# Kernel optimization log

Measured on AMD Instinct MI355X. Metric: run time of the kernel, lower is better.

Reference implementation:

```python
import jax, jax.numpy as jnp
import numpy as np

# 8 fully-diagonal directions, same order as the torch list comprehension
DIRS = [(i, j, k) for i in (-1, 1) for j in (-1, 1) for k in (-1, 1)]


def conv3d(x, w, b):
    # x: (B,Cin,D,H,W), w: (Cout,Cin,3,3,3), padding=1, stride=1
    y = jax.lax.conv_general_dilated(
        x, w, window_strides=(1, 1, 1), padding=[(1, 1)] * 3,
        dimension_numbers=('NCDHW', 'OIDHW', 'NCDHW'))
    return y + b[None, :, None, None, None]


def gru_diag_scan(z, hb, h0):
    """GruDirection3d.forward_3 with d=(1,1,1) (inputs already flipped).
    O[i,j,k] = z[i,j,k]*hb[i,j,k] + (1-z[i,j,k])*P, P = h0 if min(i,j,k)==0 else O[i-1,j-1,k-1].
    Implemented exactly as the original three slab updates per step (static slices)."""
    B, C, D, H, W = z.shape
    h = jnp.broadcast_to(h0[None, :, None, None, None].astype(z.dtype),
                         (B, C, D + 1, H + 1, W + 1))
    for ti in range(min(D, H, W)):
        a = z[:, :, ti, ti:, ti:]; g = hb[:, :, ti, ti:, ti:]
        h = h.at[:, :, ti + 1, ti + 1:, ti + 1:].set(a * g + (1 - a) * h[:, :, ti, ti:H, ti:W])
        a = z[:, :, ti + 1:, ti, ti:]; g = hb[:, :, ti + 1:, ti, ti:]
        h = h.at[:, :, ti + 2:, ti + 1, ti + 1:].set(a * g + (1 - a) * h[:, :, ti + 1:D, ti, ti:W])
        a = z[:, :, ti + 1:, ti + 1:, ti]; g = hb[:, :, ti + 1:, ti + 1:, ti]
        h = h.at[:, :, ti + 2:, ti + 2:, ti + 1].set(a * g + (1 - a) * h[:, :, ti + 1:D, ti + 1:H, ti])
    return h[:, :, 1:, 1:, 1:]


def setup_inputs() -> dict:
    key = jax.random.key(0)
    ks = jax.random.split(key, 8)
    B, Cin, Cout, D = 2, 32, 32, 32
    x = jax.random.normal(ks[0], (B, Cin, D, D, D), dtype=jnp.float32)
    s = 0.05  # keep conv pre-activations in a sane range for the sigmoids
    Wh = s * jax.random.normal(ks[1], (8, Cout, Cin, 3, 3, 3), dtype=jnp.float32)
    bh = s * jax.random.normal(ks[2], (8, Cout), dtype=jnp.float32)
    Wz = s * jax.random.normal(ks[3], (8, Cout, Cin, 3, 3, 3), dtype=jnp.float32)
    bz = s * jax.random.normal(ks[4], (8, Cout), dtype=jnp.float32)
    Ws = s * jax.random.normal(ks[5], (8, Cout, Cin, 3, 3, 3), dtype=jnp.float32)
    bs = s * jax.random.normal(ks[6], (8, Cout), dtype=jnp.float32)
    h0 = s * jax.random.normal(ks[7], (8, Cout), dtype=jnp.float32)
    return {"x": x, "Wh": Wh, "bh": bh, "Wz": Wz, "bz": bz, "Ws": Ws, "bs": bs, "h0": h0}


def reference(x, Wh, bh, Wz, bz, Ws, bs, h0):
    out = None
    for n, (di, dj, dk) in enumerate(DIRS):
        hb = conv3d(x, Wh[n], bh[n])
        z = jax.nn.sigmoid(conv3d(x, Wz[n], bz[n]))
        s = jax.nn.sigmoid(conv3d(x, Ws[n], bs[n]))
        flip_axes = tuple(ax for ax, d in zip((2, 3, 4), (di, dj, dk)) if d < 0)
        zf = jnp.flip(z, flip_axes) if flip_axes else z
        hf = jnp.flip(hb, flip_axes) if flip_axes else hb
        hout = gru_diag_scan(zf, hf, h0[n])
        hout = jnp.flip(hout, flip_axes) if flip_axes else hout
        contrib = hout * s
        out = contrib if out is None else out + contrib
    return out
```

## Files before the change

kernel.cpp:

```cpp
#include <hip/hip_runtime.h>
#include <hip/hip_bf16.h>
#include <math.h>

#define NB 2
#define NC 32
#define DD 32
#define VOL (DD*DD*DD)
#define WDIR (NC*NC*27)
#define BUF_ELEMS (NB*VOL*NC)
#define WT_DIR (27*96*32)

typedef __attribute__((ext_vector_type(8))) short short8;
typedef __attribute__((ext_vector_type(4))) float f32x4;

__device__ __forceinline__ short f2bf(float v) {
    unsigned u = __float_as_uint(v);
    unsigned r = (u + 0x7fffu + ((u >> 16) & 1u)) >> 16;
    return (short)r;
}
__device__ __forceinline__ float bf2f(short s) {
    return __uint_as_float(((unsigned)(unsigned short)s) << 16);
}
__device__ __forceinline__ float bf2f_lo(unsigned u) {
    return __uint_as_float(u << 16);
}
__device__ __forceinline__ float bf2f_hi(unsigned u) {
    return __uint_as_float(u & 0xffff0000u);
}
__device__ __forceinline__ unsigned pack2(float a, float b) {
    return ((unsigned)(unsigned short)f2bf(a)) | (((unsigned)(unsigned short)f2bf(b)) << 16);
}

__device__ __forceinline__ void async_copy16(const void* g, void* l) {
    __builtin_amdgcn_global_load_lds(
        (const __attribute__((address_space(1))) unsigned*)g,
        (__attribute__((address_space(3))) unsigned*)l, 16, 0, 0);
}

__global__ __launch_bounds__(256) void prep_xw(
    const float* __restrict__ x,
    const float* __restrict__ Wh, const float* __restrict__ Wz,
    const float* __restrict__ Ws,
    short* __restrict__ xT, short* __restrict__ Wt)
{
    __shared__ float tl[32][33];
    if (blockIdx.x < 2048) {
        const int blk = blockIdx.x;
        const int b = blk >> 10;
        const int i = (blk >> 5) & 31;
        const int j = blk & 31;

        const int k  = threadIdx.x & 31;
        const int cq = threadIdx.x >> 5;
        #pragma unroll
        for (int t = 0; t < 4; ++t) {
            const int ci = cq * 4 + t;
            tl[ci][k] = x[(((b*NC + ci)*DD + i)*DD + j)*DD + k];
        }
        __syncthreads();
        const int ci2 = threadIdx.x & 31;
        const int kq  = threadIdx.x >> 5;
        const int base = ((b*DD + i)*DD + j)*DD*NC;
        #pragma unroll
        for (int t = 0; t < 4; ++t) {
            const int kk = kq * 4 + t;
            xT[base + kk*NC + ci2] = f2bf(tl[ci2][kk]);
        }
    } else {
        const int idx = (blockIdx.x - 2048) * 256 + threadIdx.x;
        if (idx >= 8*WT_DIR) return;
        const int ci  = idx & 31;
        const int n   = (idx >> 5) % 96;
        const int tap = (idx / (96*32)) % 27;
        const int dir = idx / WT_DIR;
        const int g   = n >> 5;
        const int co  = n & 31;
        const float* W = (g == 0) ? Wh : (g == 1) ? Wz : Ws;
        Wt[idx] = f2bf(W[dir*WDIR + (co*NC + ci)*27 + tap]);
    }
}

__global__ __launch_bounds__(256, 3) void conv_mfma(
    const short* __restrict__ xT, const short* __restrict__ Wt,
    const float* __restrict__ bh, const float* __restrict__ bz,
    const float* __restrict__ bs,
    short* __restrict__ bufh, short* __restrict__ bufz, short* __restrict__ bufs)
{
    __shared__ __align__(16) short As[18*34*32];

    const int tid  = threadIdx.x;
    const int lane = tid & 63;
    const int wave = tid >> 6;
    const int mh   = wave & 1;
    const int nh   = wave >> 1;
    const int lr   = lane & 15;
    const int lq   = lane >> 4;

    const int blk = blockIdx.x;
    const int j0  = (blk & 7) * 4;
    const int i   = (blk >> 3) & 31;
    const int b   = (blk >> 8) & 1;
    const int dir = blk >> 9;

    if (tid < 144) {
        const int row = tid >> 3;
        const int e   = tid & 7;
        const int off = row*2176 + (e < 4 ? e*16 : 2112 + (e - 4)*16);
        *(short8*)((char*)As + off) = short8{};
    }
    for (int t = wave; t < 36; t += 4) {
        const int row  = t >> 1;
        const int half = t & 1;
        const int rr = row / 6, jc = row - rr*6;
        const int ii = i + rr - 1, jj = j0 + jc - 1;
        char* ldst = (char*)As + row*2176 + 64 + half*1024 + lane*16;
        if ((unsigned)ii < 32u && (unsigned)jj < 32u) {
            const char* g = (const char*)(xT + ((b*DD + ii)*DD + jj)*DD*NC)
                            + half*1024 + lane*16;
            async_copy16(g, ldst);
        } else {
            *(short8*)ldst = short8{};
        }
    }
    __syncthreads();

    const int nbase = nh*48;
    const short* __restrict__ Wd = Wt + dir*WT_DIR;

    f32x4 acc[4][3];
    #pragma unroll
    for (int nt = 0; nt < 3; ++nt) {
        #pragma unroll
        for (int r = 0; r < 4; ++r) {
            const int n = nbase + nt*16 + lq*4 + r;
            const int gg = n >> 5, co = n & 31;
            const float bv = (gg == 0) ? bh[dir*NC + co]
                           : (gg == 1) ? bz[dir*NC + co] : bs[dir*NC + co];
            #pragma unroll
            for (int mt = 0; mt < 4; ++mt) acc[mt][nt][r] = bv;
        }
    }

    #pragma unroll
    for (int g9 = 0; g9 < 9; ++g9) {
        short8 bfr[3][3];
        #pragma unroll
        for (int rk = 0; rk < 3; ++rk)
            #pragma unroll
            for (int nt = 0; nt < 3; ++nt)
                bfr[rk][nt] = *(const short8*)
                    &Wd[((g9*3 + rk)*96 + nbase + nt*16 + lr)*32 + lq*8];

        const int ri = g9 / 3;
        const int rj = g9 - 3*ri;
        const int rowb = (ri*6 + mh*2 + rj) * 1088;

        #pragma unroll
        for (int rk = 0; rk < 3; ++rk) {
            short8 afr[4];
            #pragma unroll
            for (int mt = 0; mt < 4; ++mt) {
                const int jd  = mt >> 1;
                const int kvr = (mt & 1)*16 + lr + rk;
                afr[mt] = *(const short8*)&As[rowb + jd*1088 + kvr*32 + lq*8];
            }
            #pragma unroll
            for (int mt = 0; mt < 4; ++mt)
                #pragma unroll
                for (int nt = 0; nt < 3; ++nt)
                    acc[mt][nt] = __builtin_amdgcn_mfma_f32_16x16x32_bf16(
                        bfr[rk][nt], afr[mt], acc[mt][nt], 0, 0, 0);
        }
    }

    #pragma unroll
    for (int nt = 0; nt < 3; ++nt) {
        const int n0 = nbase + nt*16 + lq*4;
        const int gg = n0 >> 5;
        const int co = n0 & 31;
        short* __restrict__ dst = ((gg == 0) ? bufh : (gg == 1) ? bufz : bufs)
                                  + (size_t)dir * BUF_ELEMS;
        #pragma unroll
        for (int mt = 0; mt < 4; ++mt) {
            const int jd = mt >> 1;
            const int kv = (mt & 1)*16 + lr;
            float v0 = acc[mt][nt][0], v1 = acc[mt][nt][1];
            float v2 = acc[mt][nt][2], v3 = acc[mt][nt][3];
            if (gg != 0) {
                v0 = 1.0f/(1.0f + __expf(-v0)); v1 = 1.0f/(1.0f + __expf(-v1));
                v2 = 1.0f/(1.0f + __expf(-v2)); v3 = 1.0f/(1.0f + __expf(-v3));
            }
            uint2 pk = { pack2(v0, v1), pack2(v2, v3) };
            *(uint2*)&dst[((((b*DD + i)*DD + (j0 + mh*2 + jd))*DD + kv)*NC) + co] = pk;
        }
    }
}

__global__ __launch_bounds__(256) void gru_scan(
    const short* __restrict__ bufh, const short* __restrict__ bufz,
    const short* __restrict__ bufs, short* __restrict__ cont,
    const float* __restrict__ h0)
{
    const int dir = blockIdx.z;
    const int di = (dir & 4) ? 1 : -1;
    const int dj = (dir & 2) ? 1 : -1;
    const int dk = (dir & 1) ? 1 : -1;
    const size_t doff = (size_t)dir * BUF_ELEMS;
    const short* __restrict__ bh_ = bufh + doff;
    const short* __restrict__ bz_ = bufz + doff;
    const short* __restrict__ bs_ = bufs + doff;
    short* __restrict__ ct_ = cont + doff;

    const int c8   = threadIdx.x & 7;
    const int slot = threadIdx.x >> 3;
    const int cid  = blockIdx.x * 32 + slot;
    if (cid >= 2977) return;
    const int b = blockIdx.y;

    int ic, jc, kc;
    if (cid < 1024)      { ic = 0;             jc = cid >> 5;      kc = cid & 31; }
    else if (cid < 2016) { int t = cid - 1024; ic = 1 + (t >> 5);  jc = 0; kc = t & 31; }
    else                 { int t = cid - 2016; int q = t / 31;
                           ic = 1 + q;         jc = 1 + (t - q*31); kc = 0; }

    int mx = ic > jc ? ic : jc; if (kc > mx) mx = kc;
    const int L  = 32 - mx;
    const int i0 = (di > 0) ? ic : 31 - ic;
    const int j0 = (dj > 0) ? jc : 31 - jc;
    const int k0 = (dk > 0) ? kc : 31 - kc;
    const int step = di*(DD*DD*NC) + dj*(DD*NC) + dk*NC;

    int p = b*(VOL*NC) + i0*(DD*DD*NC) + j0*(DD*NC) + k0*NC + c8*4;
    float p0 = h0[dir*NC + c8*4 + 0];
    float p1 = h0[dir*NC + c8*4 + 1];
    float p2 = h0[dir*NC + c8*4 + 2];
    float p3 = h0[dir*NC + c8*4 + 3];

    for (int s = 0; s < L; ++s) {
        const uint2 uz = *(const uint2*)&bz_[p];
        const uint2 uh = *(const uint2*)&bh_[p];
        const uint2 us = *(const uint2*)&bs_[p];

        const float z0 = bf2f_lo(uz.x), z1 = bf2f_hi(uz.x);
        const float z2 = bf2f_lo(uz.y), z3 = bf2f_hi(uz.y);
        const float h0v = bf2f_lo(uh.x), h1v = bf2f_hi(uh.x);
        const float h2v = bf2f_lo(uh.y), h3v = bf2f_hi(uh.y);
        const float s0 = bf2f_lo(us.x), s1 = bf2f_hi(us.x);
        const float s2 = bf2f_lo(us.y), s3 = bf2f_hi(us.y);

        const float o0 = z0*h0v + (1.0f - z0)*p0;
        const float o1 = z1*h1v + (1.0f - z1)*p1;
        const float o2 = z2*h2v + (1.0f - z2)*p2;
        const float o3 = z3*h3v + (1.0f - z3)*p3;

        uint2 pk = { pack2(o0*s0, o1*s1), pack2(o2*s2, o3*s3) };
        *(uint2*)&ct_[p] = pk;

        p0 = o0; p1 = o1; p2 = o2; p3 = o3;
        p += step;
    }
}

__global__ __launch_bounds__(256) void transpose_out(
    const short* __restrict__ contrib, float* __restrict__ out)
{
    __shared__ float tl[32][33];
    const int blk = blockIdx.x;
    const int b = blk >> 10;
    const int i = (blk >> 5) & 31;
    const int j = blk & 31;

    const int c  = threadIdx.x & 31;
    const int kq = threadIdx.x >> 5;
    const int base = ((b*DD + i)*DD + j)*DD*NC;
    #pragma unroll
    for (int t = 0; t < 4; ++t) {
        const int k = kq*4 + t;
        float s = 0.0f;
        #pragma unroll
        for (int d = 0; d < 8; ++d)
            s += bf2f(contrib[(size_t)d*BUF_ELEMS + base + k*NC + c]);
        tl[k][c] = s;
    }
    __syncthreads();

    const int k2 = threadIdx.x & 31;
    const int cq = threadIdx.x >> 5;
    const int obase = b*(NC*VOL) + i*(DD*DD) + j*DD;
    #pragma unroll
    for (int t = 0; t < 4; ++t) {
        const int co = cq*4 + t;
        out[obase + co*VOL + k2] = tl[k2][co];
    }
}

extern "C" void kernel_launch(void* const* d_in, const int* in_sizes, int n_in,
                              void* d_out, int out_size, void* d_ws, size_t ws_size,
                              hipStream_t stream)
{
    const float* x  = (const float*)d_in[0];
    const float* Wh = (const float*)d_in[1];
    const float* bh = (const float*)d_in[2];
    const float* Wz = (const float*)d_in[3];
    const float* bz = (const float*)d_in[4];
    const float* Ws = (const float*)d_in[5];
    const float* bs = (const float*)d_in[6];
    const float* h0 = (const float*)d_in[7];
    float* out = (float*)d_out;

    short* bufh = (short*)d_ws;
    short* bufz = bufh + 8*(size_t)BUF_ELEMS;
    short* bufs = bufz + 8*(size_t)BUF_ELEMS;
    short* xT   = bufs + 8*(size_t)BUF_ELEMS;
    short* Wt   = xT + BUF_ELEMS;
    short* cont = Wt + 8*(size_t)WT_DIR;

    prep_xw<<<2048 + (8*WT_DIR + 255)/256, 256, 0, stream>>>(x, Wh, Wz, Ws, xT, Wt);

    conv_mfma<<<8*NB*DD*8, 256, 0, stream>>>(xT, Wt, bh, bz, bs, bufh, bufz, bufs);

    gru_scan<<<dim3((2977 + 31)/32, NB, 8), 256, 0, stream>>>(bufh, bufz, bufs, cont, h0);

    transpose_out<<<NB*DD*DD, 256, 0, stream>>>(cont, out);
}
```

Baseline: 213.0 us.

## Switch conv to 32x32x16 MFMA with 2x4 row tiles and swizzled LDS

The implicit-GEMM conv now uses 32x32x16 bf16 MFMA instead of 16x16x32. Each block covers two i-rows by four j-rows, with each wave owning two rows across all 96 output channels. The halo tile in LDS grows to 24 rows and uses an XOR swizzle on the 16-byte chunks to avoid bank conflicts. The aim is more weight and input reuse per block and fewer halo loads per output, at the cost of more accumulator registers and a halved grid that may reduce occupancy.

After: 216.2 us. Within noise of the previous version (+1.5%).

```diff
diff --git a/kernel.cpp b/kernel.cpp
--- a/kernel.cpp
+++ b/kernel.cpp
@@ -11,7 +11,7 @@
 #define WT_DIR (27*96*32)
 
 typedef __attribute__((ext_vector_type(8))) short short8;
-typedef __attribute__((ext_vector_type(4))) float f32x4;
+typedef __attribute__((ext_vector_type(16))) float f32x16;
 
 __device__ __forceinline__ short f2bf(float v) {
     unsigned u = __float_as_uint(v);
@@ -86,112 +86,112 @@
     const float* __restrict__ bs,
     short* __restrict__ bufh, short* __restrict__ bufz, short* __restrict__ bufs)
 {
-    __shared__ __align__(16) short As[18*34*32];
+    __shared__ __align__(16) short As[24*34*32];
 
     const int tid  = threadIdx.x;
     const int lane = tid & 63;
-    const int wave = tid >> 6;
-    const int mh   = wave & 1;
-    const int nh   = wave >> 1;
-    const int lr   = lane & 15;
-    const int lq   = lane >> 4;
+    const int w    = tid >> 6;
+    const int kv   = lane & 31;
+    const int hl   = lane >> 5;
 
     const int blk = blockIdx.x;
     const int j0  = (blk & 7) * 4;
-    const int i   = (blk >> 3) & 31;
-    const int b   = (blk >> 8) & 1;
-    const int dir = blk >> 9;
-
-    if (tid < 144) {
+    const int i0  = ((blk >> 3) & 15) * 2;
+    const int b   = (blk >> 7) & 1;
+    const int dir = blk >> 8;
+
+    if (tid < 192) {
         const int row = tid >> 3;
         const int e   = tid & 7;
-        const int off = row*2176 + (e < 4 ? e*16 : 2112 + (e - 4)*16);
-        *(short8*)((char*)As + off) = short8{};
-    }
-    for (int t = wave; t < 36; t += 4) {
-        const int row  = t >> 1;
-        const int half = t & 1;
+        const int g   = (e < 4) ? e : (128 + e);
+        *(short8*)((char*)As + row*2176 + g*16) = short8{};
+    }
+    for (int t = w; t < 48; t += 4) {
+        const int row = t >> 1;
+        const int h   = t & 1;
         const int rr = row / 6, jc = row - rr*6;
-        const int ii = i + rr - 1, jj = j0 + jc - 1;
-        char* ldst = (char*)As + row*2176 + 64 + half*1024 + lane*16;
+        const int ii = i0 + rr - 1, jj = j0 + jc - 1;
+        char* ldst = (char*)As + row*2176 + (1 + 16*h)*64 + lane*16;
         if ((unsigned)ii < 32u && (unsigned)jj < 32u) {
-            const char* g = (const char*)(xT + ((b*DD + ii)*DD + jj)*DD*NC)
-                            + half*1024 + lane*16;
-            async_copy16(g, ldst);
+            const int kvs = 16*h + (lane >> 2);
+            const int cq  = (lane & 3) ^ ((kvs + 1) & 3);
+            const char* gp = (const char*)(xT + (((b*DD + ii)*DD + jj)*DD)*NC)
+                             + kvs*64 + cq*16;
+            async_copy16(gp, ldst);
         } else {
             *(short8*)ldst = short8{};
         }
     }
     __syncthreads();
 
-    const int nbase = nh*48;
-    const short* __restrict__ Wd = Wt + dir*WT_DIR;
-
-    f32x4 acc[4][3];
+    const short* __restrict__ Wb = Wt + dir*WT_DIR + kv*32 + hl*8;
+
+    f32x16 acc[2][3];
     #pragma unroll
     for (int nt = 0; nt < 3; ++nt) {
         #pragma unroll
-        for (int r = 0; r < 4; ++r) {
-            const int n = nbase + nt*16 + lq*4 + r;
-            const int gg = n >> 5, co = n & 31;
-            const float bv = (gg == 0) ? bh[dir*NC + co]
-                           : (gg == 1) ? bz[dir*NC + co] : bs[dir*NC + co];
+        for (int r = 0; r < 16; ++r) {
+            const int ch = (r & 3) + 8*(r >> 2) + 4*hl;
+            const float bv = (nt == 0) ? bh[dir*NC + ch]
+                           : (nt == 1) ? bz[dir*NC + ch] : bs[dir*NC + ch];
+            acc[0][nt][r] = bv;
+            acc[1][nt][r] = bv;
+        }
+    }
+
+    const int rid0 = w*2,     idd0 = rid0 >> 2, jd0 = rid0 & 3;
+    const int rid1 = w*2 + 1, idd1 = rid1 >> 2, jd1 = rid1 & 3;
+
+    #pragma unroll
+    for (int g9 = 0; g9 < 9; ++g9) {
+        const int ri = g9 / 3, rj = g9 - 3*ri;
+        const int arow0 = ((idd0 + ri)*6 + jd0 + rj) * 2176;
+        const int arow1 = ((idd1 + ri)*6 + jd1 + rj) * 2176;
+        #pragma unroll
+        for (int rk = 0; rk < 3; ++rk) {
+            const int kvr   = kv + rk;
+            const int kvr64 = kvr * 64;
+            const int xr    = kvr & 3;
+            const short* wp0 = Wb + (g9*3 + rk)*3072;
             #pragma unroll
-            for (int mt = 0; mt < 4; ++mt) acc[mt][nt][r] = bv;
-        }
-    }
-
-    #pragma unroll
-    for (int g9 = 0; g9 < 9; ++g9) {
-        short8 bfr[3][3];
-        #pragma unroll
-        for (int rk = 0; rk < 3; ++rk)
+            for (int kc = 0; kc < 2; ++kc) {
+                const int perm = ((kc*2 + hl) ^ xr) * 16;
+                const short8 a0 = *(const short8*)((const char*)As + arow0 + kvr64 + perm);
+                const short8 a1 = *(const short8*)((const char*)As + arow1 + kvr64 + perm);
+                const short8 b0 = *(const short8*)&wp0[kc*16];
+                const short8 b1 = *(const short8*)&wp0[1024 + kc*16];
+                const short8 b2 = *(const short8*)&wp0[2048 + kc*16];
+                acc[0][0] = __builtin_amdgcn_mfma_f32_32x32x16_bf16(b0, a0, acc[0][0], 0, 0, 0);
+                acc[1][0] = __builtin_amdgcn_mfma_f32_32x32x16_bf16(b0, a1, acc[1][0], 0, 0, 0);
+                acc[0][1] = __builtin_amdgcn_mfma_f32_32x32x16_bf16(b1, a0, acc[0][1], 0, 0, 0);
+                acc[1][1] = __builtin_amdgcn_mfma_f32_32x32x16_bf16(b1, a1, acc[1][1], 0, 0, 0);
+                acc[0][2] = __builtin_amdgcn_mfma_f32_32x32x16_bf16(b2, a0, acc[0][2], 0, 0, 0);
+                acc[1][2] = __builtin_amdgcn_mfma_f32_32x32x16_bf16(b2, a1, acc[1][2], 0, 0, 0);
+            }
+        }
+    }
+
+    #pragma unroll
+    for (int nt = 0; nt < 3; ++nt) {
+        short* __restrict__ dst = ((nt == 0) ? bufh : (nt == 1) ? bufz : bufs)
+                                  + (size_t)dir * BUF_ELEMS;
+        #pragma unroll
+        for (int mt = 0; mt < 2; ++mt) {
+            const int rid = w*2 + mt;
+            const int i = i0 + (rid >> 2);
+            const int j = j0 + (rid & 3);
+            const int base = (((b*DD + i)*DD + j)*DD + kv)*NC + 4*hl;
             #pragma unroll
-            for (int nt = 0; nt < 3; ++nt)
-                bfr[rk][nt] = *(const short8*)
-                    &Wd[((g9*3 + rk)*96 + nbase + nt*16 + lr)*32 + lq*8];
-
-        const int ri = g9 / 3;
-        const int rj = g9 - 3*ri;
-        const int rowb = (ri*6 + mh*2 + rj) * 1088;
-
-        #pragma unroll
-        for (int rk = 0; rk < 3; ++rk) {
-            short8 afr[4];
-            #pragma unroll
-            for (int mt = 0; mt < 4; ++mt) {
-                const int jd  = mt >> 1;
-                const int kvr = (mt & 1)*16 + lr + rk;
-                afr[mt] = *(const short8*)&As[rowb + jd*1088 + kvr*32 + lq*8];
+            for (int q = 0; q < 4; ++q) {
+                float v0 = acc[mt][nt][4*q + 0], v1 = acc[mt][nt][4*q + 1];
+                float v2 = acc[mt][nt][4*q + 2], v3 = acc[mt][nt][4*q + 3];
+                if (nt != 0) {
+                    v0 = 1.0f/(1.0f + __expf(-v0)); v1 = 1.0f/(1.0f + __expf(-v1));
+                    v2 = 1.0f/(1.0f + __expf(-v2)); v3 = 1.0f/(1.0f + __expf(-v3));
+                }
+                uint2 pk = { pack2(v0, v1), pack2(v2, v3) };
+                *(uint2*)&dst[base + 8*q] = pk;
             }
-            #pragma unroll
-            for (int mt = 0; mt < 4; ++mt)
-                #pragma unroll
-                for (int nt = 0; nt < 3; ++nt)
-                    acc[mt][nt] = __builtin_amdgcn_mfma_f32_16x16x32_bf16(
-                        bfr[rk][nt], afr[mt], acc[mt][nt], 0, 0, 0);
-        }
-    }
-
-    #pragma unroll
-    for (int nt = 0; nt < 3; ++nt) {
-        const int n0 = nbase + nt*16 + lq*4;
-        const int gg = n0 >> 5;
-        const int co = n0 & 31;
-        short* __restrict__ dst = ((gg == 0) ? bufh : (gg == 1) ? bufz : bufs)
-                                  + (size_t)dir * BUF_ELEMS;
-        #pragma unroll
-        for (int mt = 0; mt < 4; ++mt) {
-            const int jd = mt >> 1;
-            const int kv = (mt & 1)*16 + lr;
-            float v0 = acc[mt][nt][0], v1 = acc[mt][nt][1];
-            float v2 = acc[mt][nt][2], v3 = acc[mt][nt][3];
-            if (gg != 0) {
-                v0 = 1.0f/(1.0f + __expf(-v0)); v1 = 1.0f/(1.0f + __expf(-v1));
-                v2 = 1.0f/(1.0f + __expf(-v2)); v3 = 1.0f/(1.0f + __expf(-v3));
-            }
-            uint2 pk = { pack2(v0, v1), pack2(v2, v3) };
-            *(uint2*)&dst[((((b*DD + i)*DD + (j0 + mh*2 + jd))*DD + kv)*NC) + co] = pk;
         }
     }
 }
@@ -317,7 +317,7 @@
 
     prep_xw<<<2048 + (8*WT_DIR + 255)/256, 256, 0, stream>>>(x, Wh, Wz, Ws, xT, Wt);
 
-    conv_mfma<<<8*NB*DD*8, 256, 0, stream>>>(xT, Wt, bh, bz, bs, bufh, bufz, bufs);
+    conv_mfma<<<2048, 256, 0, stream>>>(xT, Wt, bh, bz, bs, bufh, bufz, bufs);
 
     gru_scan<<<dim3((2977 + 31)/32, NB, 8), 256, 0, stream>>>(bufh, bufz, bufs, cont, h0);
 
```
